# Kernel tuning notes

Measured on AMD Instinct MI355X. Metric: run time of the kernel, lower is better.

Reference implementation:

```python
import jax, jax.numpy as jnp
import numpy as np

N_NODES = 100000
N_EDGES = 1_600_000
NFEAT, NHID, NCLASS = 256, 128, 64


def setup_inputs() -> dict:
    key = jax.random.key(0)
    ks = jax.random.split(key, 6)
    x = jax.random.normal(ks[0], (N_NODES, NFEAT), dtype=jnp.float32)
    W1 = jax.random.normal(ks[1], (NFEAT, NHID), dtype=jnp.float32) * (1.0 / np.sqrt(NFEAT))
    W2 = jax.random.normal(ks[2], (NHID, NCLASS), dtype=jnp.float32) * (1.0 / np.sqrt(NHID))
    edge_vals = jax.random.uniform(ks[3], (N_EDGES,), dtype=jnp.float32)
    edge_src = jax.random.randint(ks[4], (N_EDGES,), 0, N_NODES, dtype=jnp.int32)
    edge_dst = jax.random.randint(ks[5], (N_EDGES,), 0, N_NODES, dtype=jnp.int32)
    return {"x": x, "W1": W1, "W2": W2, "edge_vals": edge_vals,
            "edge_src": edge_src, "edge_dst": edge_dst}


def _spmm(edge_vals, edge_src, edge_dst, dense, n_nodes):
    # out[dst] += val * dense[src]  (COO sparse-matrix x dense-matrix)
    msgs = edge_vals[:, None] * dense[edge_src]  # [E, d]
    return jax.ops.segment_sum(msgs, edge_dst, num_segments=n_nodes)


def reference(x, W1, W2, edge_vals, edge_src, edge_dst):
    n = x.shape[0]
    # GraphConvolution 1: support = x @ W1; out = spmm(adj, support); relu
    h = jax.nn.relu(_spmm(edge_vals, edge_src, edge_dst, x @ W1, n))
    # GraphConvolution 2: identity activation
    mu = _spmm(edge_vals, edge_src, edge_dst, h @ W2, n)
    return mu
```

## Files before the change

kernel.cpp:

```cpp
#include <hip/hip_runtime.h>

constexpr int NFEAT  = 256;
constexpr int NHID   = 128;
constexpr int NCLASS = 64;

typedef __attribute__((ext_vector_type(8))) short short8;
typedef __attribute__((ext_vector_type(4))) float floatx4;

__device__ __forceinline__ unsigned short f2bf(float x) {
    unsigned u = __float_as_uint(x);
    u += 0x7FFFu + ((u >> 16) & 1u);
    return (unsigned short)(u >> 16);
}
__device__ __forceinline__ float bf_lo(unsigned int p) { return __uint_as_float(p << 16); }
__device__ __forceinline__ float bf_hi(unsigned int p) { return __uint_as_float(p & 0xFFFF0000u); }

constexpr int EPB = 8192;
constexpr int CAP = 8192;

__global__ __launch_bounds__(256) void init_cast_kernel(
    const float* __restrict__ W1, const float* __restrict__ W2,
    unsigned short* __restrict__ W1T, unsigned short* __restrict__ W2T,
    int* __restrict__ bcur, int nbuk)
{
    if (blockIdx.x == 0) {
        for (int b = threadIdx.x; b < nbuk; b += 256) bcur[b] = b * CAP;
        return;
    }
    int i = ((int)blockIdx.x - 1) * 256 + threadIdx.x;
    if (i < NFEAT * NHID) {
        int k = i >> 7, n = i & 127;
        W1T[n * NFEAT + k] = f2bf(W1[i]);
    }
    if (i < NHID * NCLASS) {
        int k = i >> 6, n = i & 63;
        W2T[n * NHID + k] = f2bf(W2[i]);
    }
}

__global__ __launch_bounds__(256) void gemm1_scatter_fused_kernel(
    const float* __restrict__ A,
    const unsigned short* __restrict__ BT,
    unsigned short* __restrict__ C,
    int M,
    const float* __restrict__ vals, const int* __restrict__ src,
    const int* __restrict__ dst, int* __restrict__ bcur,
    int2* __restrict__ tmp, int E, int sgrid)
{
    constexpr int KTOT = NFEAT, BN = NHID;
    constexpr int NB  = BN / 16;
    constexpr int LDA = 72;
    __shared__ unsigned short smem[64 * LDA + BN * LDA];

    if ((int)blockIdx.x < sgrid) {
        int* cnt  = reinterpret_cast<int*>(smem);
        int* base = cnt + 512;
        for (int i = threadIdx.x; i < 512; i += 256) cnt[i] = 0;
        __syncthreads();
        int begin = blockIdx.x * EPB;
        int endi = begin + EPB; if (endi > E) endi = E;
        for (int i = begin + threadIdx.x; i < endi; i += 256)
            atomicAdd(&cnt[dst[i] >> 8], 1);
        __syncthreads();
        for (int b = threadIdx.x; b < 512; b += 256) {
            int c = cnt[b];
            base[b] = c ? atomicAdd(&bcur[b], c) : 0;
            cnt[b] = 0;
        }
        __syncthreads();
        for (int i = begin + threadIdx.x; i < endi; i += 256) {
            int d = dst[i];
            int b = d >> 8;
            int pos = base[b] + atomicAdd(&cnt[b], 1);
            tmp[pos] = make_int2(src[i] | ((d & 255) << 17), __float_as_int(vals[i]));
        }
        return;
    }

    unsigned short* As = smem;
    unsigned short* Bs = smem + 64 * LDA;
    const int tid = threadIdx.x;
    const int w   = tid >> 6;
    const int l   = tid & 63;
    const int row0 = ((int)blockIdx.x - sgrid) * 64;

    floatx4 acc[NB];
    #pragma unroll
    for (int i = 0; i < NB; ++i) acc[i] = (floatx4){0.f, 0.f, 0.f, 0.f};

    for (int k0 = 0; k0 < KTOT; k0 += 64) {
        #pragma unroll
        for (int i = 0; i < 4; ++i) {
            int c = tid + 256 * i;
            int r = c >> 4, k4 = (c & 15) * 4;
            int row = row0 + r;
            float4 v = (row < M) ? *reinterpret_cast<const float4*>(A + (size_t)row * KTOT + k0 + k4)
                                 : make_float4(0.f, 0.f, 0.f, 0.f);
            ushort4 b;
            b.x = f2bf(v.x); b.y = f2bf(v.y); b.z = f2bf(v.z); b.w = f2bf(v.w);
            *reinterpret_cast<ushort4*>(&As[r * LDA + k4]) = b;
        }
        #pragma unroll
        for (int i = 0; i < BN * 8 / 256; ++i) {
            int c = tid + 256 * i;
            int n = c >> 3, k8 = (c & 7) * 8;
            uint4 v = *reinterpret_cast<const uint4*>(BT + (size_t)n * KTOT + k0 + k8);
            *reinterpret_cast<uint4*>(&Bs[n * LDA + k8]) = v;
        }
        __syncthreads();
        #pragma unroll
        for (int ks = 0; ks < 2; ++ks) {
            short8 a = *reinterpret_cast<const short8*>(&As[(16 * w + (l & 15)) * LDA + ks * 32 + (l >> 4) * 8]);
            #pragma unroll
            for (int nb = 0; nb < NB; ++nb) {
                short8 b = *reinterpret_cast<const short8*>(&Bs[(16 * nb + (l & 15)) * LDA + ks * 32 + (l >> 4) * 8]);
                acc[nb] = __builtin_amdgcn_mfma_f32_16x16x32_bf16(a, b, acc[nb], 0, 0, 0);
            }
        }
        __syncthreads();
    }
    const int cr = (l >> 4) * 4;
    const int cc = l & 15;
    #pragma unroll
    for (int nb = 0; nb < NB; ++nb) {
        #pragma unroll
        for (int r = 0; r < 4; ++r) {
            int row = row0 + 16 * w + cr + r;
            if (row < M) C[(size_t)row * BN + 16 * nb + cc] = f2bf(acc[nb][r]);
        }
    }
}

__global__ __launch_bounds__(256) void bucket_fine_kernel(
    const int* __restrict__ bcur,
    const int2* __restrict__ tmp,
    int* __restrict__ row_beg, int* __restrict__ row_end,
    int2* __restrict__ pairs, int M)
{
    __shared__ int cnt[256];
    __shared__ int excl[256];
    __shared__ int cur[256];
    const int b = blockIdx.x;
    const int beg = b * CAP, endi = bcur[b];
    const int t = threadIdx.x;
    cnt[t] = 0;
    __syncthreads();
    for (int j = beg + t; j < endi; j += 256)
        atomicAdd(&cnt[(tmp[j].x >> 17) & 255], 1);
    __syncthreads();
    int v = cnt[t];
    excl[t] = v;
    __syncthreads();
    for (int off = 1; off < 256; off <<= 1) {
        int u = (t >= off) ? excl[t - off] : 0;
        __syncthreads();
        excl[t] += u;
        __syncthreads();
    }
    int ex = excl[t] - v;
    excl[t] = ex;
    cur[t] = 0;
    int row = (b << 8) + t;
    if (row < M) { row_beg[row] = beg + ex; row_end[row] = beg + ex + v; }
    __syncthreads();
    for (int j = beg + t; j < endi; j += 256) {
        int2 p = tmp[j];
        int dl = (p.x >> 17) & 255;
        int pos = beg + excl[dl] + atomicAdd(&cur[dl], 1);
        pairs[pos] = p;
    }
}

__global__ __launch_bounds__(256) void spmm_gemm2_fused_kernel(
    const int*  __restrict__ row_beg,
    const int*  __restrict__ row_end,
    const int2* __restrict__ pairs,
    const unsigned short* __restrict__ dense,
    const unsigned short* __restrict__ W2T,
    unsigned short*       __restrict__ sup2,
    int M)
{
    __shared__ unsigned short hs[16 * 128];
    const int wv = threadIdx.x >> 6, l = threadIdx.x & 63;
    const int g = l >> 4, t = l & 15;
    const int row = blockIdx.x * 16 + wv * 4 + g;
    int beg = 0, end = 0;
    if (row < M) { beg = row_beg[row]; end = row_end[row]; }
    const uint4* d4 = reinterpret_cast<const uint4*>(dense);
    float2 a0 = {0.f, 0.f}, a1 = {0.f, 0.f}, a2 = {0.f, 0.f}, a3 = {0.f, 0.f};
    int j = beg;
    for (; j + 4 <= end; j += 4) {
        int2 p0 = pairs[j], p1 = pairs[j + 1], p2 = pairs[j + 2], p3 = pairs[j + 3];
        uint4 x0 = d4[(size_t)(p0.x & 0x1FFFF) * 16 + t];
        uint4 x1 = d4[(size_t)(p1.x & 0x1FFFF) * 16 + t];
        uint4 x2 = d4[(size_t)(p2.x & 0x1FFFF) * 16 + t];
        uint4 x3 = d4[(size_t)(p3.x & 0x1FFFF) * 16 + t];
        float v0 = __int_as_float(p0.y), v1 = __int_as_float(p1.y);
        float v2 = __int_as_float(p2.y), v3 = __int_as_float(p3.y);
        a0.x += v0 * bf_lo(x0.x); a0.y += v0 * bf_hi(x0.x);
        a1.x += v0 * bf_lo(x0.y); a1.y += v0 * bf_hi(x0.y);
        a2.x += v0 * bf_lo(x0.z); a2.y += v0 * bf_hi(x0.z);
        a3.x += v0 * bf_lo(x0.w); a3.y += v0 * bf_hi(x0.w);
        a0.x += v1 * bf_lo(x1.x); a0.y += v1 * bf_hi(x1.x);
        a1.x += v1 * bf_lo(x1.y); a1.y += v1 * bf_hi(x1.y);
        a2.x += v1 * bf_lo(x1.z); a2.y += v1 * bf_hi(x1.z);
        a3.x += v1 * bf_lo(x1.w); a3.y += v1 * bf_hi(x1.w);
        a0.x += v2 * bf_lo(x2.x); a0.y += v2 * bf_hi(x2.x);
        a1.x += v2 * bf_lo(x2.y); a1.y += v2 * bf_hi(x2.y);
        a2.x += v2 * bf_lo(x2.z); a2.y += v2 * bf_hi(x2.z);
        a3.x += v2 * bf_lo(x2.w); a3.y += v2 * bf_hi(x2.w);
        a0.x += v3 * bf_lo(x3.x); a0.y += v3 * bf_hi(x3.x);
        a1.x += v3 * bf_lo(x3.y); a1.y += v3 * bf_hi(x3.y);
        a2.x += v3 * bf_lo(x3.z); a2.y += v3 * bf_hi(x3.z);
        a3.x += v3 * bf_lo(x3.w); a3.y += v3 * bf_hi(x3.w);
    }
    for (; j < end; ++j) {
        int2 p = pairs[j];
        uint4 x = d4[(size_t)(p.x & 0x1FFFF) * 16 + t];
        float v = __int_as_float(p.y);
        a0.x += v * bf_lo(x.x); a0.y += v * bf_hi(x.x);
        a1.x += v * bf_lo(x.y); a1.y += v * bf_hi(x.y);
        a2.x += v * bf_lo(x.z); a2.y += v * bf_hi(x.z);
        a3.x += v * bf_lo(x.w); a3.y += v * bf_hi(x.w);
    }
    {
        uint4 o;
        o.x = (unsigned)f2bf(fmaxf(a0.x, 0.f)) | ((unsigned)f2bf(fmaxf(a0.y, 0.f)) << 16);
        o.y = (unsigned)f2bf(fmaxf(a1.x, 0.f)) | ((unsigned)f2bf(fmaxf(a1.y, 0.f)) << 16);
        o.z = (unsigned)f2bf(fmaxf(a2.x, 0.f)) | ((unsigned)f2bf(fmaxf(a2.y, 0.f)) << 16);
        o.w = (unsigned)f2bf(fmaxf(a3.x, 0.f)) | ((unsigned)f2bf(fmaxf(a3.y, 0.f)) << 16);
        const int rloc = wv * 4 + g;
        const int byte = (t * 16) ^ ((rloc & 7) << 4);
        *reinterpret_cast<uint4*>(reinterpret_cast<char*>(hs) + rloc * 256 + byte) = o;
    }
    __syncthreads();
    floatx4 acc = (floatx4){0.f, 0.f, 0.f, 0.f};
    const int lr = l & 15, lk = l >> 4;
    #pragma unroll
    for (int ks = 0; ks < 4; ++ks) {
        const int byte = (ks * 64 + lk * 16) ^ ((lr & 7) << 4);
        short8 a = *reinterpret_cast<const short8*>(reinterpret_cast<const char*>(hs) + lr * 256 + byte);
        short8 b = *reinterpret_cast<const short8*>(W2T + (size_t)(wv * 16 + lr) * NHID + ks * 32 + lk * 8);
        acc = __builtin_amdgcn_mfma_f32_16x16x32_bf16(a, b, acc, 0, 0, 0);
    }
    const int cr = lk * 4, cc = lr;
    #pragma unroll
    for (int q = 0; q < 4; ++q) {
        int orow = blockIdx.x * 16 + cr + q;
        if (orow < M) sup2[(size_t)orow * NCLASS + wv * 16 + cc] = f2bf(acc[q]);
    }
}

__global__ __launch_bounds__(256) void spmm_gather64_kernel(
    const int*  __restrict__ row_beg,
    const int*  __restrict__ row_end,
    const int2* __restrict__ pairs,
    const unsigned short* __restrict__ dense,
    float*                __restrict__ out,
    int M)
{
    const int wv = threadIdx.x >> 6, l = threadIdx.x & 63;
    const int g = l >> 3, t = l & 7;
    const int row = blockIdx.x * 32 + wv * 8 + g;
    int beg = 0, end = 0;
    if (row < M) { beg = row_beg[row]; end = row_end[row]; }
    const uint4* d4 = reinterpret_cast<const uint4*>(dense);
    float2 a0 = {0.f, 0.f}, a1 = {0.f, 0.f}, a2 = {0.f, 0.f}, a3 = {0.f, 0.f};
    int j = beg;
    for (; j + 4 <= end; j += 4) {
        int2 p0 = pairs[j], p1 = pairs[j + 1], p2 = pairs[j + 2], p3 = pairs[j + 3];
        uint4 x0 = d4[(size_t)(p0.x & 0x1FFFF) * 8 + t];
        uint4 x1 = d4[(size_t)(p1.x & 0x1FFFF) * 8 + t];
        uint4 x2 = d4[(size_t)(p2.x & 0x1FFFF) * 8 + t];
        uint4 x3 = d4[(size_t)(p3.x & 0x1FFFF) * 8 + t];
        float v0 = __int_as_float(p0.y), v1 = __int_as_float(p1.y);
        float v2 = __int_as_float(p2.y), v3 = __int_as_float(p3.y);
        a0.x += v0 * bf_lo(x0.x); a0.y += v0 * bf_hi(x0.x);
        a1.x += v0 * bf_lo(x0.y); a1.y += v0 * bf_hi(x0.y);
        a2.x += v0 * bf_lo(x0.z); a2.y += v0 * bf_hi(x0.z);
        a3.x += v0 * bf_lo(x0.w); a3.y += v0 * bf_hi(x0.w);
        a0.x += v1 * bf_lo(x1.x); a0.y += v1 * bf_hi(x1.x);
        a1.x += v1 * bf_lo(x1.y); a1.y += v1 * bf_hi(x1.y);
        a2.x += v1 * bf_lo(x1.z); a2.y += v1 * bf_hi(x1.z);
        a3.x += v1 * bf_lo(x1.w); a3.y += v1 * bf_hi(x1.w);
        a0.x += v2 * bf_lo(x2.x); a0.y += v2 * bf_hi(x2.x);
        a1.x += v2 * bf_lo(x2.y); a1.y += v2 * bf_hi(x2.y);
        a2.x += v2 * bf_lo(x2.z); a2.y += v2 * bf_hi(x2.z);
        a3.x += v2 * bf_lo(x2.w); a3.y += v2 * bf_hi(x2.w);
        a0.x += v3 * bf_lo(x3.x); a0.y += v3 * bf_hi(x3.x);
        a1.x += v3 * bf_lo(x3.y); a1.y += v3 * bf_hi(x3.y);
        a2.x += v3 * bf_lo(x3.z); a2.y += v3 * bf_hi(x3.z);
        a3.x += v3 * bf_lo(x3.w); a3.y += v3 * bf_hi(x3.w);
    }
    for (; j < end; ++j) {
        int2 p = pairs[j];
        uint4 x = d4[(size_t)(p.x & 0x1FFFF) * 8 + t];
        float v = __int_as_float(p.y);
        a0.x += v * bf_lo(x.x); a0.y += v * bf_hi(x.x);
        a1.x += v * bf_lo(x.y); a1.y += v * bf_hi(x.y);
        a2.x += v * bf_lo(x.z); a2.y += v * bf_hi(x.z);
        a3.x += v * bf_lo(x.w); a3.y += v * bf_hi(x.w);
    }
    if (row < M) {
        float4 o0 = make_float4(a0.x, a0.y, a1.x, a1.y);
        float4 o1 = make_float4(a2.x, a2.y, a3.x, a3.y);
        float4* op = reinterpret_cast<float4*>(out + (size_t)row * 64 + t * 8);
        op[0] = o0;
        op[1] = o1;
    }
}

extern "C" void kernel_launch(void* const* d_in, const int* in_sizes, int n_in,
                              void* d_out, int out_size, void* d_ws, size_t ws_size,
                              hipStream_t stream) {
    const float* x  = (const float*)d_in[0];
    const float* W1 = (const float*)d_in[1];
    const float* W2 = (const float*)d_in[2];
    const float* ev = (const float*)d_in[3];
    const int*   es = (const int*)d_in[4];
    const int*   ed = (const int*)d_in[5];
    float* out = (float*)d_out;

    const int M = in_sizes[0] / NFEAT;
    const int E = in_sizes[3];
    const int nbuk = (M + 255) >> 8;

    size_t off = 0;
    auto alloc = [&](size_t bytes) -> void* {
        void* p = (char*)d_ws + off;
        off += (bytes + 255) & ~(size_t)255;
        return p;
    };
    unsigned short* sup_bf  = (unsigned short*)alloc((size_t)M * NHID * 2);
    unsigned short* sup2_bf = (unsigned short*)alloc((size_t)M * NCLASS * 2);
    unsigned short* W1T     = (unsigned short*)alloc((size_t)NHID * NFEAT * 2);
    unsigned short* W2T     = (unsigned short*)alloc((size_t)NCLASS * NHID * 2);
    int*  row_beg = (int*) alloc((size_t)M * sizeof(int));
    int*  row_end = (int*) alloc((size_t)M * sizeof(int));
    int*  bcur    = (int*) alloc(512 * sizeof(int));
    int2* tmp     = (int2*)alloc((size_t)nbuk * CAP * sizeof(int2));
    int2* pairs   = (int2*)alloc((size_t)nbuk * CAP * sizeof(int2));
    (void)ws_size;

    const int pgrid = (E + EPB - 1) / EPB;
    const int castg = (NFEAT * NHID + 255) / 256;
    const int g1grid = (M + 63) / 64;

    init_cast_kernel<<<castg + 1, 256, 0, stream>>>(W1, W2, W1T, W2T, bcur, nbuk);

    gemm1_scatter_fused_kernel<<<pgrid + g1grid, 256, 0, stream>>>(
        x, W1T, sup_bf, M, ev, es, ed, bcur, tmp, E, pgrid);

    bucket_fine_kernel<<<nbuk, 256, 0, stream>>>(bcur, tmp, row_beg, row_end, pairs, M);

    spmm_gemm2_fused_kernel<<<(M + 15) / 16, 256, 0, stream>>>(
        row_beg, row_end, pairs, sup_bf, W2T, sup2_bf, M);

    spmm_gather64_kernel<<<(M + 31) / 32, 256, 0, stream>>>(
        row_beg, row_end, pairs, sup2_bf, out, M);
}
```

Baseline: 165.0 us.

## Pre-cast x to bf16 and fuse bucket fine-sort into GEMM1 launch

The coarse edge scatter moves into a prep kernel that also casts x to bf16 and transposes the weights, with bcur zeroed by a memset and bucket bases computed as b<<13. GEMM1 then loads bf16 A directly and runs alongside the per-bucket fine sort in one launch, removing a separate kernel launch and the per-tile fp32-to-bf16 conversion. This costs an extra 51MB bf16 copy of x written and read back. When the workspace is too small, pairs aliases xbf and the unfused path is kept.

```diff
diff --git a/kernel.cpp b/kernel.cpp
--- a/kernel.cpp
+++ b/kernel.cpp
@@ -18,71 +18,133 @@
 constexpr int EPB = 8192;
 constexpr int CAP = 8192;
 
-__global__ __launch_bounds__(256) void init_cast_kernel(
+__global__ __launch_bounds__(256) void prep_fused_kernel(
+    const float* __restrict__ x,
     const float* __restrict__ W1, const float* __restrict__ W2,
+    unsigned short* __restrict__ xbf,
     unsigned short* __restrict__ W1T, unsigned short* __restrict__ W2T,
-    int* __restrict__ bcur, int nbuk)
-{
-    if (blockIdx.x == 0) {
-        for (int b = threadIdx.x; b < nbuk; b += 256) bcur[b] = b * CAP;
-        return;
-    }
-    int i = ((int)blockIdx.x - 1) * 256 + threadIdx.x;
-    if (i < NFEAT * NHID) {
-        int k = i >> 7, n = i & 127;
-        W1T[n * NFEAT + k] = f2bf(W1[i]);
-    }
-    if (i < NHID * NCLASS) {
-        int k = i >> 6, n = i & 63;
-        W2T[n * NHID + k] = f2bf(W2[i]);
-    }
-}
-
-__global__ __launch_bounds__(256) void gemm1_scatter_fused_kernel(
-    const float* __restrict__ A,
+    const float* __restrict__ vals, const int* __restrict__ src,
+    const int* __restrict__ dst, int* __restrict__ bcur,
+    int2* __restrict__ tmp, int E, int M, int sgrid, int cxgrid)
+{
+    __shared__ int smem[1024];
+    const int bid = blockIdx.x, tid = threadIdx.x;
+    if (bid < sgrid) {
+        int* cnt  = smem;
+        int* base = smem + 512;
+        for (int i = tid; i < 512; i += 256) cnt[i] = 0;
+        __syncthreads();
+        int begin = bid * EPB;
+        int endi = begin + EPB; if (endi > E) endi = E;
+        for (int i = begin + tid; i < endi; i += 256)
+            atomicAdd(&cnt[dst[i] >> 8], 1);
+        __syncthreads();
+        for (int b = tid; b < 512; b += 256) {
+            int c = cnt[b];
+            base[b] = c ? atomicAdd(&bcur[b], c) : 0;
+            cnt[b] = 0;
+        }
+        __syncthreads();
+        for (int i = begin + tid; i < endi; i += 256) {
+            int d = dst[i];
+            int b = d >> 8;
+            int pos = (b << 13) + base[b] + atomicAdd(&cnt[b], 1);
+            tmp[pos] = make_int2(src[i] | ((d & 255) << 17), __float_as_int(vals[i]));
+        }
+    } else if (bid < sgrid + cxgrid) {
+        const int blk = bid - sgrid;
+        const float4* in4 = reinterpret_cast<const float4*>(x);
+        uint4* o4 = reinterpret_cast<uint4*>(xbf);
+        const long total8 = (long)M * NFEAT / 8;
+        #pragma unroll
+        for (int i = 0; i < 2; ++i) {
+            long oidx = (long)blk * 512 + i * 256 + tid;
+            if (oidx < total8) {
+                float4 a = in4[oidx * 2], b = in4[oidx * 2 + 1];
+                uint4 u;
+                u.x = (unsigned)f2bf(a.x) | ((unsigned)f2bf(a.y) << 16);
+                u.y = (unsigned)f2bf(a.z) | ((unsigned)f2bf(a.w) << 16);
+                u.z = (unsigned)f2bf(b.x) | ((unsigned)f2bf(b.y) << 16);
+                u.w = (unsigned)f2bf(b.z) | ((unsigned)f2bf(b.w) << 16);
+                o4[oidx] = u;
+            }
+        }
+    } else {
+        int i = (bid - sgrid - cxgrid) * 256 + tid;
+        if (i < NFEAT * NHID) {
+            int k = i >> 7, n = i & 127;
+            W1T[n * NFEAT + k] = f2bf(W1[i]);
+        }
+        if (i < NHID * NCLASS) {
+            int k = i >> 6, n = i & 63;
+            W2T[n * NHID + k] = f2bf(W2[i]);
+        }
+    }
+}
+
+__device__ __forceinline__ void fine_body(
+    int b, int tid, int* cnt, int* excl, int* cur,
+    const int* __restrict__ bcur, const int2* __restrict__ tmp,
+    int* __restrict__ row_beg, int* __restrict__ row_end,
+    int2* __restrict__ pairs, int M)
+{
+    const int beg = b * CAP;
+    int c0 = bcur[b]; if (c0 > CAP) c0 = CAP;
+    const int endi = beg + c0;
+    cnt[tid] = 0;
+    __syncthreads();
+    for (int j = beg + tid; j < endi; j += 256)
+        atomicAdd(&cnt[(tmp[j].x >> 17) & 255], 1);
+    __syncthreads();
+    int v = cnt[tid];
+    excl[tid] = v;
+    __syncthreads();
+    for (int off = 1; off < 256; off <<= 1) {
+        int u = (tid >= off) ? excl[tid - off] : 0;
+        __syncthreads();
+        excl[tid] += u;
+        __syncthreads();
+    }
+    int ex = excl[tid] - v;
+    excl[tid] = ex;
+    cur[tid] = 0;
+    int row = (b << 8) + tid;
+    if (row < M) { row_beg[row] = beg + ex; row_end[row] = beg + ex + v; }
+    __syncthreads();
+    for (int j = beg + tid; j < endi; j += 256) {
+        int2 p = tmp[j];
+        int dl = (p.x >> 17) & 255;
+        int pos = beg + excl[dl] + atomicAdd(&cur[dl], 1);
+        pairs[pos] = p;
+    }
+}
+
+__global__ __launch_bounds__(256) void gemm1_fine_fused_kernel(
+    const unsigned short* __restrict__ A,
     const unsigned short* __restrict__ BT,
     unsigned short* __restrict__ C,
     int M,
-    const float* __restrict__ vals, const int* __restrict__ src,
-    const int* __restrict__ dst, int* __restrict__ bcur,
-    int2* __restrict__ tmp, int E, int sgrid)
+    const int* __restrict__ bcur, const int2* __restrict__ tmp,
+    int* __restrict__ row_beg, int* __restrict__ row_end,
+    int2* __restrict__ pairs, int fgrid)
 {
     constexpr int KTOT = NFEAT, BN = NHID;
     constexpr int NB  = BN / 16;
     constexpr int LDA = 72;
     __shared__ unsigned short smem[64 * LDA + BN * LDA];
 
-    if ((int)blockIdx.x < sgrid) {
+    const int tid = threadIdx.x;
+    if ((int)blockIdx.x < fgrid) {
         int* cnt  = reinterpret_cast<int*>(smem);
-        int* base = cnt + 512;
-        for (int i = threadIdx.x; i < 512; i += 256) cnt[i] = 0;
-        __syncthreads();
-        int begin = blockIdx.x * EPB;
-        int endi = begin + EPB; if (endi > E) endi = E;
-        for (int i = begin + threadIdx.x; i < endi; i += 256)
-            atomicAdd(&cnt[dst[i] >> 8], 1);
-        __syncthreads();
-        for (int b = threadIdx.x; b < 512; b += 256) {
-            int c = cnt[b];
-            base[b] = c ? atomicAdd(&bcur[b], c) : 0;
-            cnt[b] = 0;
-        }
-        __syncthreads();
-        for (int i = begin + threadIdx.x; i < endi; i += 256) {
-            int d = dst[i];
-            int b = d >> 8;
-            int pos = base[b] + atomicAdd(&cnt[b], 1);
-            tmp[pos] = make_int2(src[i] | ((d & 255) << 17), __float_as_int(vals[i]));
-        }
+        fine_body(blockIdx.x, tid, cnt, cnt + 256, cnt + 512,
+                  bcur, tmp, row_beg, row_end, pairs, M);
         return;
     }
 
     unsigned short* As = smem;
     unsigned short* Bs = smem + 64 * LDA;
-    const int tid = threadIdx.x;
-    const int w   = tid >> 6;
-    const int l   = tid & 63;
-    const int row0 = ((int)blockIdx.x - sgrid) * 64;
+    const int w = tid >> 6, l = tid & 63;
+    const int row0 = ((int)blockIdx.x - fgrid) * 64;
 
     floatx4 acc[NB];
     #pragma unroll
@@ -90,15 +152,13 @@
 
     for (int k0 = 0; k0 < KTOT; k0 += 64) {
         #pragma unroll
-        for (int i = 0; i < 4; ++i) {
+        for (int i = 0; i < 2; ++i) {
             int c = tid + 256 * i;
-            int r = c >> 4, k4 = (c & 15) * 4;
+            int r = c >> 3, k8 = (c & 7) * 8;
             int row = row0 + r;
-            float4 v = (row < M) ? *reinterpret_cast<const float4*>(A + (size_t)row * KTOT + k0 + k4)
-                                 : make_float4(0.f, 0.f, 0.f, 0.f);
-            ushort4 b;
-            b.x = f2bf(v.x); b.y = f2bf(v.y); b.z = f2bf(v.z); b.w = f2bf(v.w);
-            *reinterpret_cast<ushort4*>(&As[r * LDA + k4]) = b;
+            uint4 v = (row < M) ? *reinterpret_cast<const uint4*>(A + (size_t)row * KTOT + k0 + k8)
+                                : make_uint4(0u, 0u, 0u, 0u);
+            *reinterpret_cast<uint4*>(&As[r * LDA + k8]) = v;
         }
         #pragma unroll
         for (int i = 0; i < BN * 8 / 256; ++i) {
@@ -132,43 +192,13 @@
 }
 
 __global__ __launch_bounds__(256) void bucket_fine_kernel(
-    const int* __restrict__ bcur,
-    const int2* __restrict__ tmp,
+    const int* __restrict__ bcur, const int2* __restrict__ tmp,
     int* __restrict__ row_beg, int* __restrict__ row_end,
     int2* __restrict__ pairs, int M)
 {
-    __shared__ int cnt[256];
-    __shared__ int excl[256];
-    __shared__ int cur[256];
-    const int b = blockIdx.x;
-    const int beg = b * CAP, endi = bcur[b];
-    const int t = threadIdx.x;
-    cnt[t] = 0;
-    __syncthreads();
-    for (int j = beg + t; j < endi; j += 256)
-        atomicAdd(&cnt[(tmp[j].x >> 17) & 255], 1);
-    __syncthreads();
-    int v = cnt[t];
-    excl[t] = v;
-    __syncthreads();
-    for (int off = 1; off < 256; off <<= 1) {
-        int u = (t >= off) ? excl[t - off] : 0;
-        __syncthreads();
-        excl[t] += u;
-        __syncthreads();
-    }
-    int ex = excl[t] - v;
-    excl[t] = ex;
-    cur[t] = 0;
-    int row = (b << 8) + t;
-    if (row < M) { row_beg[row] = beg + ex; row_end[row] = beg + ex + v; }
-    __syncthreads();
-    for (int j = beg + t; j < endi; j += 256) {
-        int2 p = tmp[j];
-        int dl = (p.x >> 17) & 255;
-        int pos = beg + excl[dl] + atomicAdd(&cur[dl], 1);
-        pairs[pos] = p;
-    }
+    __shared__ int smem[768];
+    fine_body(blockIdx.x, threadIdx.x, smem, smem + 256, smem + 512,
+              bcur, tmp, row_beg, row_end, pairs, M);
 }
 
 __global__ __launch_bounds__(256) void spmm_gemm2_fused_kernel(
@@ -331,6 +361,7 @@
         off += (bytes + 255) & ~(size_t)255;
         return p;
     };
+    unsigned short* xbf     = (unsigned short*)alloc((size_t)M * NFEAT * 2);
     unsigned short* sup_bf  = (unsigned short*)alloc((size_t)M * NHID * 2);
     unsigned short* sup2_bf = (unsigned short*)alloc((size_t)M * NCLASS * 2);
     unsigned short* W1T     = (unsigned short*)alloc((size_t)NHID * NFEAT * 2);
@@ -339,19 +370,30 @@
     int*  row_end = (int*) alloc((size_t)M * sizeof(int));
     int*  bcur    = (int*) alloc(512 * sizeof(int));
     int2* tmp     = (int2*)alloc((size_t)nbuk * CAP * sizeof(int2));
-    int2* pairs   = (int2*)alloc((size_t)nbuk * CAP * sizeof(int2));
-    (void)ws_size;
-
-    const int pgrid = (E + EPB - 1) / EPB;
-    const int castg = (NFEAT * NHID + 255) / 256;
+
+    const size_t pairs_bytes = (size_t)nbuk * CAP * sizeof(int2);
+    const bool big_ws = (off + pairs_bytes + 256 <= ws_size);
+    int2* pairs = big_ws ? (int2*)alloc(pairs_bytes) : (int2*)xbf;
+
+    const int sgrid  = (E + EPB - 1) / EPB;
+    const int cxgrid = (M * NFEAT + 4095) / 4096;
+    const int cwgrid = (NFEAT * NHID + 255) / 256;
+    const int fgrid  = nbuk;
     const int g1grid = (M + 63) / 64;
 
-    init_cast_kernel<<<castg + 1, 256, 0, stream>>>(W1, W2, W1T, W2T, bcur, nbuk);
-
-    gemm1_scatter_fused_kernel<<<pgrid + g1grid, 256, 0, stream>>>(
-        x, W1T, sup_bf, M, ev, es, ed, bcur, tmp, E, pgrid);
-
-    bucket_fine_kernel<<<nbuk, 256, 0, stream>>>(bcur, tmp, row_beg, row_end, pairs, M);
+    hipMemsetAsync(bcur, 0, 512 * sizeof(int), stream);
+
+    prep_fused_kernel<<<sgrid + cxgrid + cwgrid, 256, 0, stream>>>(
+        x, W1, W2, xbf, W1T, W2T, ev, es, ed, bcur, tmp, E, M, sgrid, cxgrid);
+
+    if (big_ws) {
+        gemm1_fine_fused_kernel<<<fgrid + g1grid, 256, 0, stream>>>(
+            xbf, W1T, sup_bf, M, bcur, tmp, row_beg, row_end, pairs, fgrid);
+    } else {
+        gemm1_fine_fused_kernel<<<g1grid, 256, 0, stream>>>(
+            xbf, W1T, sup_bf, M, bcur, tmp, row_beg, row_end, pairs, 0);
+        bucket_fine_kernel<<<nbuk, 256, 0, stream>>>(bcur, tmp, row_beg, row_end, pairs, M);
+    }
 
     spmm_gemm2_fused_kernel<<<(M + 15) / 16, 256, 0, stream>>>(
         row_beg, row_end, pairs, sup_bf, W2T, sup2_bf, M);
```

New measurement: 199.9 us. 21.2% more time.

## Double-buffer B via direct global-to-LDS loads, read A straight to registers

Applied to the files above, without the earlier changes.

Restructures the GEMM1 part of the fused kernel. A rows are now loaded directly from global memory into registers and converted to bf16 there, so A no longer passes through shared memory. The W1T tile is double-buffered in LDS using global_load_lds with an XOR-swizzled layout, so the next k-tile loads while the current one computes and bank conflicts are avoided. The trade-off is that A global loads are less coalesced (each lane reads 32 bytes from its own row) and the LDS footprint grows to two 16 KB B buffers, which may lower occupancy.

```diff
diff --git a/kernel.cpp b/kernel.cpp
--- a/kernel.cpp
+++ b/kernel.cpp
@@ -14,6 +14,12 @@
 }
 __device__ __forceinline__ float bf_lo(unsigned int p) { return __uint_as_float(p << 16); }
 __device__ __forceinline__ float bf_hi(unsigned int p) { return __uint_as_float(p & 0xFFFF0000u); }
+
+__device__ __forceinline__ void gload16(const void* g, void* l) {
+    __builtin_amdgcn_global_load_lds(
+        (const __attribute__((address_space(1))) void*)g,
+        (__attribute__((address_space(3))) void*)l, 16, 0, 0);
+}
 
 constexpr int EPB = 8192;
 constexpr int CAP = 8192;
@@ -48,27 +54,26 @@
     int2* __restrict__ tmp, int E, int sgrid)
 {
     constexpr int KTOT = NFEAT, BN = NHID;
-    constexpr int NB  = BN / 16;
-    constexpr int LDA = 72;
-    __shared__ unsigned short smem[64 * LDA + BN * LDA];
-
+    __shared__ unsigned short smem[2 * BN * 64];
+
+    const int tid = threadIdx.x;
     if ((int)blockIdx.x < sgrid) {
         int* cnt  = reinterpret_cast<int*>(smem);
         int* base = cnt + 512;
-        for (int i = threadIdx.x; i < 512; i += 256) cnt[i] = 0;
+        for (int i = tid; i < 512; i += 256) cnt[i] = 0;
         __syncthreads();
         int begin = blockIdx.x * EPB;
         int endi = begin + EPB; if (endi > E) endi = E;
-        for (int i = begin + threadIdx.x; i < endi; i += 256)
+        for (int i = begin + tid; i < endi; i += 256)
             atomicAdd(&cnt[dst[i] >> 8], 1);
         __syncthreads();
-        for (int b = threadIdx.x; b < 512; b += 256) {
+        for (int b = tid; b < 512; b += 256) {
             int c = cnt[b];
             base[b] = c ? atomicAdd(&bcur[b], c) : 0;
             cnt[b] = 0;
         }
         __syncthreads();
-        for (int i = begin + threadIdx.x; i < endi; i += 256) {
+        for (int i = begin + tid; i < endi; i += 256) {
             int d = dst[i];
             int b = d >> 8;
             int pos = base[b] + atomicAdd(&cnt[b], 1);
@@ -77,52 +82,58 @@
         return;
     }
 
-    unsigned short* As = smem;
-    unsigned short* Bs = smem + 64 * LDA;
-    const int tid = threadIdx.x;
-    const int w   = tid >> 6;
-    const int l   = tid & 63;
+    const int w = tid >> 6, l = tid & 63;
+    const int lr = l & 15, lk = l >> 4;
     const int row0 = ((int)blockIdx.x - sgrid) * 64;
-
-    floatx4 acc[NB];
+    const int ra = row0 + 16 * w + lr;
+    const float* Arow = A + (size_t)((ra < M) ? ra : (M - 1)) * KTOT;
+
+    const char* BTb = (const char*)BT;
+    char* Bb = (char*)smem;
+    auto stageB = [&](int buf, int kt) {
+        #pragma unroll
+        for (int j = 0; j < 4; ++j) {
+            int i = w * 4 + j;
+            int r = i * 8 + (l >> 3);
+            int chunk = (l & 7) ^ (l >> 3);
+            gload16(BTb + (size_t)r * (KTOT * 2) + kt * 128 + chunk * 16,
+                    Bb + buf * 16384 + i * 1024);
+        }
+    };
+
+    floatx4 acc[8];
     #pragma unroll
-    for (int i = 0; i < NB; ++i) acc[i] = (floatx4){0.f, 0.f, 0.f, 0.f};
-
-    for (int k0 = 0; k0 < KTOT; k0 += 64) {
-        #pragma unroll
-        for (int i = 0; i < 4; ++i) {
-            int c = tid + 256 * i;
-            int r = c >> 4, k4 = (c & 15) * 4;
-            int row = row0 + r;
-            float4 v = (row < M) ? *reinterpret_cast<const float4*>(A + (size_t)row * KTOT + k0 + k4)
-                                 : make_float4(0.f, 0.f, 0.f, 0.f);
-            ushort4 b;
-            b.x = f2bf(v.x); b.y = f2bf(v.y); b.z = f2bf(v.z); b.w = f2bf(v.w);
-            *reinterpret_cast<ushort4*>(&As[r * LDA + k4]) = b;
-        }
-        #pragma unroll
-        for (int i = 0; i < BN * 8 / 256; ++i) {
-            int c = tid + 256 * i;
-            int n = c >> 3, k8 = (c & 7) * 8;
-            uint4 v = *reinterpret_cast<const uint4*>(BT + (size_t)n * KTOT + k0 + k8);
-            *reinterpret_cast<uint4*>(&Bs[n * LDA + k8]) = v;
-        }
-        __syncthreads();
+    for (int i = 0; i < 8; ++i) acc[i] = (floatx4){0.f, 0.f, 0.f, 0.f};
+
+    stageB(0, 0);
+    __syncthreads();
+    int cur = 0;
+    for (int kt = 0; kt < 4; ++kt) {
+        if (kt < 3) stageB(cur ^ 1, kt + 1);
         #pragma unroll
         for (int ks = 0; ks < 2; ++ks) {
-            short8 a = *reinterpret_cast<const short8*>(&As[(16 * w + (l & 15)) * LDA + ks * 32 + (l >> 4) * 8]);
+            const float* ap = Arow + kt * 64 + ks * 32 + lk * 8;
+            float4 v0 = *reinterpret_cast<const float4*>(ap);
+            float4 v1 = *reinterpret_cast<const float4*>(ap + 4);
+            short8 a;
+            a[0] = (short)f2bf(v0.x); a[1] = (short)f2bf(v0.y);
+            a[2] = (short)f2bf(v0.z); a[3] = (short)f2bf(v0.w);
+            a[4] = (short)f2bf(v1.x); a[5] = (short)f2bf(v1.y);
+            a[6] = (short)f2bf(v1.z); a[7] = (short)f2bf(v1.w);
             #pragma unroll
-            for (int nb = 0; nb < NB; ++nb) {
-                short8 b = *reinterpret_cast<const short8*>(&Bs[(16 * nb + (l & 15)) * LDA + ks * 32 + (l >> 4) * 8]);
+            for (int nb = 0; nb < 8; ++nb) {
+                int rb = nb * 16 + lr;
+                int byteo = cur * 16384 + rb * 128 + (((ks * 4 + lk) ^ (lr & 7)) << 4);
+                short8 b = *reinterpret_cast<const short8*>(Bb + byteo);
                 acc[nb] = __builtin_amdgcn_mfma_f32_16x16x32_bf16(a, b, acc[nb], 0, 0, 0);
             }
         }
         __syncthreads();
-    }
-    const int cr = (l >> 4) * 4;
-    const int cc = l & 15;
+        cur ^= 1;
+    }
+    const int cr = lk * 4, cc = lr;
     #pragma unroll
-    for (int nb = 0; nb < NB; ++nb) {
+    for (int nb = 0; nb < 8; ++nb) {
         #pragma unroll
         for (int r = 0; r < 4; ++r) {
             int row = row0 + 16 * w + cr + r;
```

New measurement: 165.3 us. Within noise of the previous version (+0.2%).

## Split fused SpMM+GEMM2 into column-sliced gather kernel and separate GEMM

Applied to the files above, without the earlier changes.

Replaces the fused SpMM-plus-GEMM2 kernel with two kernels. The first gathers 128-wide rows in 8 column slices, one slice per block, with each lane handling one 16-byte chunk for one row, and writes the relu'd hidden state to a new bf16 buffer. The second is a standalone MFMA GEMM over 64-row tiles. The slicing is meant to shrink the gathered working set per block so the gathered rows stay in cache. The cost is an extra round trip of the hidden matrix through global memory, an extra launch, and each block re-reading the pairs list once per slice.

```diff
diff --git a/kernel.cpp b/kernel.cpp
--- a/kernel.cpp
+++ b/kernel.cpp
@@ -171,30 +171,31 @@
     }
 }
 
-__global__ __launch_bounds__(256) void spmm_gemm2_fused_kernel(
+__global__ __launch_bounds__(256) void spmm_gather128_sliced_kernel(
     const int*  __restrict__ row_beg,
     const int*  __restrict__ row_end,
     const int2* __restrict__ pairs,
     const unsigned short* __restrict__ dense,
-    const unsigned short* __restrict__ W2T,
-    unsigned short*       __restrict__ sup2,
+    unsigned short*       __restrict__ hout,
     int M)
 {
-    __shared__ unsigned short hs[16 * 128];
+    const int s  = blockIdx.x & 7;
+    const int rb = blockIdx.x >> 3;
     const int wv = threadIdx.x >> 6, l = threadIdx.x & 63;
-    const int g = l >> 4, t = l & 15;
-    const int row = blockIdx.x * 16 + wv * 4 + g;
+    const int p  = l >> 1, half = l & 1;
+    const int row = rb * 128 + wv * 32 + p;
     int beg = 0, end = 0;
     if (row < M) { beg = row_beg[row]; end = row_end[row]; }
     const uint4* d4 = reinterpret_cast<const uint4*>(dense);
+    const int co = s * 2 + half;
     float2 a0 = {0.f, 0.f}, a1 = {0.f, 0.f}, a2 = {0.f, 0.f}, a3 = {0.f, 0.f};
     int j = beg;
     for (; j + 4 <= end; j += 4) {
         int2 p0 = pairs[j], p1 = pairs[j + 1], p2 = pairs[j + 2], p3 = pairs[j + 3];
-        uint4 x0 = d4[(size_t)(p0.x & 0x1FFFF) * 16 + t];
-        uint4 x1 = d4[(size_t)(p1.x & 0x1FFFF) * 16 + t];
-        uint4 x2 = d4[(size_t)(p2.x & 0x1FFFF) * 16 + t];
-        uint4 x3 = d4[(size_t)(p3.x & 0x1FFFF) * 16 + t];
+        uint4 x0 = d4[(size_t)(p0.x & 0x1FFFF) * 16 + co];
+        uint4 x1 = d4[(size_t)(p1.x & 0x1FFFF) * 16 + co];
+        uint4 x2 = d4[(size_t)(p2.x & 0x1FFFF) * 16 + co];
+        uint4 x3 = d4[(size_t)(p3.x & 0x1FFFF) * 16 + co];
         float v0 = __int_as_float(p0.y), v1 = __int_as_float(p1.y);
         float v2 = __int_as_float(p2.y), v3 = __int_as_float(p3.y);
         a0.x += v0 * bf_lo(x0.x); a0.y += v0 * bf_hi(x0.x);
@@ -215,39 +216,82 @@
         a3.x += v3 * bf_lo(x3.w); a3.y += v3 * bf_hi(x3.w);
     }
     for (; j < end; ++j) {
-        int2 p = pairs[j];
-        uint4 x = d4[(size_t)(p.x & 0x1FFFF) * 16 + t];
-        float v = __int_as_float(p.y);
+        int2 pp = pairs[j];
+        uint4 x = d4[(size_t)(pp.x & 0x1FFFF) * 16 + co];
+        float v = __int_as_float(pp.y);
         a0.x += v * bf_lo(x.x); a0.y += v * bf_hi(x.x);
         a1.x += v * bf_lo(x.y); a1.y += v * bf_hi(x.y);
         a2.x += v * bf_lo(x.z); a2.y += v * bf_hi(x.z);
         a3.x += v * bf_lo(x.w); a3.y += v * bf_hi(x.w);
     }
-    {
+    if (row < M) {
         uint4 o;
         o.x = (unsigned)f2bf(fmaxf(a0.x, 0.f)) | ((unsigned)f2bf(fmaxf(a0.y, 0.f)) << 16);
         o.y = (unsigned)f2bf(fmaxf(a1.x, 0.f)) | ((unsigned)f2bf(fmaxf(a1.y, 0.f)) << 16);
         o.z = (unsigned)f2bf(fmaxf(a2.x, 0.f)) | ((unsigned)f2bf(fmaxf(a2.y, 0.f)) << 16);
         o.w = (unsigned)f2bf(fmaxf(a3.x, 0.f)) | ((unsigned)f2bf(fmaxf(a3.y, 0.f)) << 16);
-        const int rloc = wv * 4 + g;
-        const int byte = (t * 16) ^ ((rloc & 7) << 4);
-        *reinterpret_cast<uint4*>(reinterpret_cast<char*>(hs) + rloc * 256 + byte) = o;
-    }
-    __syncthreads();
-    floatx4 acc = (floatx4){0.f, 0.f, 0.f, 0.f};
-    const int lr = l & 15, lk = l >> 4;
+        reinterpret_cast<uint4*>(hout)[(size_t)row * 16 + co] = o;
+    }
+}
+
+__global__ __launch_bounds__(256) void gemm2_kernel(
+    const unsigned short* __restrict__ A,
+    const unsigned short* __restrict__ BT,
+    unsigned short* __restrict__ C,
+    int M)
+{
+    constexpr int KTOT = NHID, BN = NCLASS;
+    constexpr int NB  = BN / 16;
+    constexpr int LDA = 72;
+    __shared__ unsigned short As[64 * LDA];
+    __shared__ unsigned short Bs[BN * LDA];
+    const int tid = threadIdx.x;
+    const int w   = tid >> 6;
+    const int l   = tid & 63;
+    const int row0 = blockIdx.x * 64;
+
+    floatx4 acc[NB];
     #pragma unroll
-    for (int ks = 0; ks < 4; ++ks) {
-        const int byte = (ks * 64 + lk * 16) ^ ((lr & 7) << 4);
-        short8 a = *reinterpret_cast<const short8*>(reinterpret_cast<const char*>(hs) + lr * 256 + byte);
-        short8 b = *reinterpret_cast<const short8*>(W2T + (size_t)(wv * 16 + lr) * NHID + ks * 32 + lk * 8);
-        acc = __builtin_amdgcn_mfma_f32_16x16x32_bf16(a, b, acc, 0, 0, 0);
-    }
-    const int cr = lk * 4, cc = lr;
+    for (int i = 0; i < NB; ++i) acc[i] = (floatx4){0.f, 0.f, 0.f, 0.f};
+
+    for (int k0 = 0; k0 < KTOT; k0 += 64) {
+        #pragma unroll
+        for (int i = 0; i < 2; ++i) {
+            int c = tid + 256 * i;
+            int r = c >> 3, k8 = (c & 7) * 8;
+            int row = row0 + r;
+            uint4 v = (row < M) ? *reinterpret_cast<const uint4*>(A + (size_t)row * KTOT + k0 + k8)
+                                : make_uint4(0u, 0u, 0u, 0u);
+            *reinterpret_cast<uint4*>(&As[r * LDA + k8]) = v;
+        }
+        #pragma unroll
+        for (int i = 0; i < BN * 8 / 256; ++i) {
+            int c = tid + 256 * i;
+            int n = c >> 3, k8 = (c & 7) * 8;
+            uint4 v = *reinterpret_cast<const uint4*>(BT + (size_t)n * KTOT + k0 + k8);
+            *reinterpret_cast<uint4*>(&Bs[n * LDA + k8]) = v;
+        }
+        __syncthreads();
+        #pragma unroll
+        for (int ks = 0; ks < 2; ++ks) {
+            short8 a = *reinterpret_cast<const short8*>(&As[(16 * w + (l & 15)) * LDA + ks * 32 + (l >> 4) * 8]);
+            #pragma unroll
+            for (int nb = 0; nb < NB; ++nb) {
+                short8 b = *reinterpret_cast<const short8*>(&Bs[(16 * nb + (l & 15)) * LDA + ks * 32 + (l >> 4) * 8]);
+                acc[nb] = __builtin_amdgcn_mfma_f32_16x16x32_bf16(a, b, acc[nb], 0, 0, 0);
+            }
+        }
+        __syncthreads();
+    }
+    const int cr = (l >> 4) * 4;
+    const int cc = l & 15;
     #pragma unroll
-    for (int q = 0; q < 4; ++q) {
-        int orow = blockIdx.x * 16 + cr + q;
-        if (orow < M) sup2[(size_t)orow * NCLASS + wv * 16 + cc] = f2bf(acc[q]);
+    for (int nb = 0; nb < NB; ++nb) {
+        #pragma unroll
+        for (int r = 0; r < 4; ++r) {
+            int row = row0 + 16 * w + cr + r;
+            if (row < M) C[(size_t)row * BN + 16 * nb + cc] = f2bf(acc[nb][r]);
+        }
     }
 }
 
@@ -332,6 +376,7 @@
         return p;
     };
     unsigned short* sup_bf  = (unsigned short*)alloc((size_t)M * NHID * 2);
+    unsigned short* h_bf    = (unsigned short*)alloc((size_t)M * NHID * 2);
     unsigned short* sup2_bf = (unsigned short*)alloc((size_t)M * NCLASS * 2);
     unsigned short* W1T     = (unsigned short*)alloc((size_t)NHID * NFEAT * 2);
     unsigned short* W2T     = (unsigned short*)alloc((size_t)NCLASS * NHID * 2);
@@ -345,6 +390,7 @@
     const int pgrid = (E + EPB - 1) / EPB;
     const int castg = (NFEAT * NHID + 255) / 256;
     const int g1grid = (M + 63) / 64;
+    const int rbgrid = (M + 127) / 128;
 
     init_cast_kernel<<<castg + 1, 256, 0, stream>>>(W1, W2, W1T, W2T, bcur, nbuk);
 
@@ -353,8 +399,10 @@
 
     bucket_fine_kernel<<<nbuk, 256, 0, stream>>>(bcur, tmp, row_beg, row_end, pairs, M);
 
-    spmm_gemm2_fused_kernel<<<(M + 15) / 16, 256, 0, stream>>>(
-        row_beg, row_end, pairs, sup_bf, W2T, sup2_bf, M);
+    spmm_gather128_sliced_kernel<<<rbgrid * 8, 256, 0, stream>>>(
+        row_beg, row_end, pairs, sup_bf, h_bf, M);
+
+    gemm2_kernel<<<(M + 63) / 64, 256, 0, stream>>>(h_bf, W2T, sup2_bf, M);
 
     spmm_gather64_kernel<<<(M + 31) / 32, 256, 0, stream>>>(
         row_beg, row_end, pairs, sup2_bf, out, M);
```

New measurement: 366.9 us. +122.4%, slower.
